# Performance work log

Measured on AMD Instinct MI355X. Metric: run time of the kernel, lower is better.

## Reference

```python
import jax, jax.numpy as jnp
import numpy as np

Q8 = 127.0   # 2**7 - 1
Q4 = 7.0     # 2**3 - 1
EPS = 1e-5
NEG = -1e9


def _quant_absmax_last(t, qmax=Q8):
    # smoothquant-style per-token / per-out-channel fake quant (clamp BEFORE div)
    scales = jnp.maximum(jnp.max(jnp.abs(t), axis=-1, keepdims=True), EPS) / qmax
    return jnp.round(t / scales) * scales


def _w8a8_linear(x, w, b, quantize_output=False):
    # W8A8Linear: 8-bit per-token act fake quant, 8-bit per-channel weight fake quant
    y = jnp.einsum('bte,oe->bto', _quant_absmax_last(x), _quant_absmax_last(w)) + b
    return _quant_absmax_last(y) if quantize_output else y


def _fake_quant_mix(t):
    # fake_quant_mix: xmax = abs().amax(-1, keepdim)[0] -> drops batch dim (uses batch-0 scales)
    xmax = jnp.max(jnp.abs(t), axis=-1, keepdims=True)[0]  # [T,1]
    scales = jnp.maximum(xmax / Q8, EPS)                   # clamp AFTER div here
    return jnp.round(t / scales) * scales


def _fake_quant_k4(t):
    # fake_quant: 4-bit, per last dim
    scales = jnp.maximum(jnp.max(jnp.abs(t), axis=-1, keepdims=True), EPS) / Q4
    return jnp.round(t / scales) * scales


def _fake_quant_v8(t):
    # fake_quant_v: 8-bit, axis=-2 (per channel over sequence)
    scales = jnp.maximum(jnp.max(jnp.abs(t), axis=-2, keepdims=True), EPS) / Q8
    return jnp.round(t / scales) * scales


def setup_inputs() -> dict:
    key = jax.random.key(0)
    ks = jax.random.split(key, 9)
    B, T, E = 1, 2048, 2048
    hidden_states = jax.random.normal(ks[0], (B, T, E), jnp.float32)
    causal = jnp.triu(jnp.full((T, T), NEG, jnp.float32), k=1)
    attention_mask = jnp.broadcast_to(causal[None, None], (B, 1, T, T))

    def lin(k):
        kw, kb = jax.random.split(k)
        w = jax.random.normal(kw, (E, E), jnp.float32) * (E ** -0.5)
        b = jax.random.normal(kb, (E,), jnp.float32) * 0.02
        return w, b

    q_w, q_b = lin(ks[1])
    k_w, k_b = lin(ks[2])
    v_w, v_b = lin(ks[3])
    o_w, o_b = lin(ks[4])
    return dict(hidden_states=hidden_states, attention_mask=attention_mask,
                q_w=q_w, q_b=q_b, k_w=k_w, k_b=k_b, v_w=v_w, v_b=v_b,
                o_w=o_w, o_b=o_b, num_heads=16)


def reference(hidden_states, attention_mask, q_w, q_b, k_w, k_b, v_w, v_b, o_w, o_b, num_heads):
    B, T, E = hidden_states.shape
    H = num_heads
    D = E // H
    scaling = D ** -0.5

    q = _w8a8_linear(hidden_states, q_w, q_b) * scaling                  # [B,T,E]
    k = _w8a8_linear(hidden_states, k_w, k_b)                            # [B,T,E]
    v = _w8a8_linear(hidden_states, v_w, v_b, quantize_output=True)      # [B,T,E]

    def to_heads(t):
        return t.reshape(B, T, H, D).transpose(0, 2, 1, 3).reshape(B * H, T, D)

    q1 = to_heads(q)
    k1 = to_heads(k)

    # ---- pass 1: heavy-hitter accumulated attention score ----
    aw = jnp.einsum('btd,bsd->bts', q1, k1)                               # [B*H,T,T]
    aw = aw.reshape(B, H, T, T) + attention_mask
    aw = jnp.maximum(aw, jnp.finfo(aw.dtype).min).reshape(B * H, T, T)
    tmp_attn = jax.nn.softmax(aw, axis=-1)
    acc = tmp_attn.sum(axis=-2).sum(axis=0)[None]                         # [1,T]
    heavy_budget = T
    row_vector = (heavy_budget - jnp.arange(heavy_budget, dtype=jnp.float32))[None]
    acc = acc / row_vector / (B * H)

    # grouped top-k over 4 equal score ranges
    ratios = [0.25, 0.25, 0.25, 0.25]
    k_top = int(heavy_budget / 40)
    idx_list = []
    start = 1
    for i, r in enumerate(ratios):
        rs = int(heavy_budget * r)
        end = min(start + rs - 1, heavy_budget) if i < len(ratios) - 1 else heavy_budget
        part = acc[:, start - 1:end]
        _, ti = jax.lax.top_k(part, k_top)
        idx_list.append(ti + (start - 1))
        start = end + 1
    topk_idx = jnp.concatenate(idx_list, axis=-1).reshape(-1)             # [4*k_top]

    # ---- mixed-precision KV fake quantization ----
    k_imp = _fake_quant_mix(k)        # 8-bit keys for important tokens
    k_low = _fake_quant_k4(k)         # 4-bit keys elsewhere
    k_mixed = k_low.at[:, topk_idx, :].set(k_imp[:, topk_idx, :])
    v_q = _fake_quant_v8(v)

    k2 = to_heads(k_mixed)
    v2 = to_heads(v_q)

    # ---- pass 2: real attention ----
    aw2 = jnp.einsum('btd,bsd->bts', q1, k2).reshape(B, H, T, T) + attention_mask
    probs = jax.nn.softmax(aw2.reshape(B * H, T, T), axis=-1)
    ctx = jnp.einsum('bts,bsd->btd', probs, v2)                           # [B*H,T,D]
    ctx = ctx.reshape(B, H, T, D).transpose(0, 2, 1, 3).reshape(B, T, E)
    return _w8a8_linear(ctx, o_w, o_b)
```

## Files before the change

kernel.cpp:

```cpp
#include <hip/hip_runtime.h>
#include <stdint.h>

#define TT 2048
#define EE 2048
#define HH 16
#define DD 128

static constexpr float F_EPS = 1e-5f;
static constexpr float F_SCALING = (float)0.08838834764831845;

using f32x4  = __attribute__((ext_vector_type(4))) float;
using bf16x8 = __attribute__((ext_vector_type(8))) short;
using u16x8  = __attribute__((ext_vector_type(8))) unsigned short;
using i32x4  = __attribute__((ext_vector_type(4))) int;

#define MFMA_BF16(a,b,c) __builtin_amdgcn_mfma_f32_16x16x32_bf16((a),(b),(c),0,0,0)
#define MFMA_I8(a,b,c)   __builtin_amdgcn_mfma_i32_16x16x64_i8((a),(b),(c),0,0,0)

#define GLD16(gp, lp) __builtin_amdgcn_global_load_lds( \
    (__attribute__((address_space(1))) void*)(unsigned long long)(gp), \
    (__attribute__((address_space(3))) void*)(lp), 16, 0, 0)

__device__ __forceinline__ unsigned short f2bf(float x){
  unsigned u = __float_as_uint(x);
  u = (u + 0x7FFFu + ((u >> 16) & 1u)) >> 16;
  return (unsigned short)u;
}
__device__ __forceinline__ float bf2f(unsigned short h){
  return __uint_as_float(((unsigned)h) << 16);
}
__device__ __forceinline__ float blockmax(float am, float* red, int tid){
  __syncthreads();
  #pragma unroll
  for (int o=1;o<64;o<<=1) am = fmaxf(am, __shfl_xor(am, o));
  if ((tid&63)==0) red[tid>>6] = am;
  __syncthreads();
  return fmaxf(fmaxf(red[0],red[1]), fmaxf(red[2],red[3]));
}

__device__ __forceinline__ void cid_map(int cid, int& qt, int& ch, int& nc){
  if (cid < 8)       { qt = cid;                ch = 0;            nc = 1; }
  else if (cid < 24) { qt = 8  + ((cid-8)>>1);  ch = (cid-8)&1;    nc = 2; }
  else if (cid < 48) { qt = 16 + (cid-24)/3;    ch = (cid-24)%3;   nc = 3; }
  else               { qt = 24 + ((cid-48)>>2); ch = (cid-48)&3;   nc = 4; }
}
__device__ __forceinline__ int aoff(int qt){
  return (qt<16) ? 2*(qt-8) : ((qt<24) ? 16+3*(qt-16) : 40+4*(qt-24));
}
__device__ __forceinline__ int aoff2(int qt){
  return (qt<16) ? (qt-8) : ((qt<24) ? 8+2*(qt-16) : 24+3*(qt-24));
}
__device__ __forceinline__ void attn_remap(int& h, int& cid){
  const int flat = blockIdx.y*80 + blockIdx.x;
  const int j = flat & 15;
  h = (j & 7)*2 + (j >> 3);
  cid = flat >> 4;
}

__device__ __forceinline__ void stage_k64x128(const unsigned short* gbase, unsigned short* lds, int tid){
  const char* gb = (const char*)gbase;
  char* lb = (char*)lds;
  #pragma unroll
  for (int i=0;i<4;i++){
    const int idx = i*256 + tid;
    const int r = idx >> 4, c = idx & 15;
    GLD16(gb + (size_t)r*(EE*2) + (unsigned)((c*16) ^ ((r&7)<<4)), lb + idx*16);
  }
}
__device__ __forceinline__ void stage_v128x64(const unsigned short* gbase, unsigned short* lds, int tid){
  const char* gb = (const char*)gbase;
  char* lb = (char*)lds;
  #pragma unroll
  for (int i=0;i<4;i++){
    const int idx = i*256 + tid;
    const int r = idx >> 3, c = idx & 7;
    GLD16(gb + (size_t)r*(TT*2) + (unsigned)((c*16) ^ ((r&7)<<4)), lb + idx*16);
  }
}
__device__ __forceinline__ bf16x8 frag_k(const unsigned short* lds, int kr, int dbyte){
  return *(const bf16x8*)((const char*)lds + kr*256 + (dbyte ^ ((kr&7)<<4)));
}
__device__ __forceinline__ bf16x8 frag_v(const unsigned short* lds, int dr, int kbyte){
  return *(const bf16x8*)((const char*)lds + dr*128 + (kbyte ^ ((dr&7)<<4)));
}

__global__ __launch_bounds__(256) void k_quant5(
    const float* __restrict__ hs, const float* __restrict__ qwf,
    const float* __restrict__ kwf, const float* __restrict__ vwf,
    const float* __restrict__ owf,
    char* __restrict__ qx, char* __restrict__ qw4,
    float* __restrict__ sx, float* __restrict__ sw)
{
  __shared__ float red[4];
  const int which = blockIdx.x >> 11;
  const int row = blockIdx.x & (TT-1);
  const int tid = threadIdx.x;
  const float* in; char* outq; float* outs;
  if      (which==0){ in=hs;  outq=qx;                   outs=sx;      }
  else if (which==1){ in=qwf; outq=qw4;                  outs=sw;      }
  else if (which==2){ in=kwf; outq=qw4+(size_t)EE*EE;    outs=sw+EE;   }
  else if (which==3){ in=vwf; outq=qw4+(size_t)2*EE*EE;  outs=sw+2*EE; }
  else              { in=owf; outq=qw4+(size_t)3*EE*EE;  outs=sw+3*EE; }
  const float* r = in + (size_t)row * EE;
  float x[8];
  {
    const f32x4 a = *(const f32x4*)(r + tid*8);
    const f32x4 b = *(const f32x4*)(r + tid*8 + 4);
    x[0]=a[0]; x[1]=a[1]; x[2]=a[2]; x[3]=a[3];
    x[4]=b[0]; x[5]=b[1]; x[6]=b[2]; x[7]=b[3];
  }
  float am = 0.f;
  #pragma unroll
  for (int j=0;j<8;j++) am = fmaxf(am, fabsf(x[j]));
  am = blockmax(am, red, tid);
  const float s = fmaxf(am, F_EPS) / 127.f;
  if (tid==0) outs[row] = s;
  union { char c[8]; int2 v; } u;
  #pragma unroll
  for (int j=0;j<8;j++) u.c[j] = (char)(int)rintf(x[j]/s);
  *(int2*)(outq + (size_t)row*EE + tid*8) = u.v;
}

__global__ __launch_bounds__(256) void k_rowquant8(
    const float* __restrict__ in, char* __restrict__ outq, float* __restrict__ outs)
{
  __shared__ float red[4];
  const int row = blockIdx.x;
  const int tid = threadIdx.x;
  const float* r = in + (size_t)row * EE;
  float x[8];
  {
    const f32x4 a = *(const f32x4*)(r + tid*8);
    const f32x4 b = *(const f32x4*)(r + tid*8 + 4);
    x[0]=a[0]; x[1]=a[1]; x[2]=a[2]; x[3]=a[3];
    x[4]=b[0]; x[5]=b[1]; x[6]=b[2]; x[7]=b[3];
  }
  float am = 0.f;
  #pragma unroll
  for (int j=0;j<8;j++) am = fmaxf(am, fabsf(x[j]));
  am = blockmax(am, red, tid);
  const float s = fmaxf(am, F_EPS) / 127.f;
  if (tid==0) outs[row] = s;
  union { char c[8]; int2 v; } u;
  #pragma unroll
  for (int j=0;j<8;j++) u.c[j] = (char)(int)rintf(x[j]/s);
  *(int2*)(outq + (size_t)row*EE + tid*8) = u.v;
}

__global__ __launch_bounds__(256) void k_quant_kmixed(
    const float* __restrict__ kin, const int* __restrict__ imp,
    unsigned short* __restrict__ qkm, float* __restrict__ sk,
    float* __restrict__ kmn)
{
  __shared__ float red[4];
  const int row = blockIdx.x;
  const int tid = threadIdx.x;
  const float* r = kin + (size_t)row * EE;
  float x[8];
  {
    const f32x4 a = *(const f32x4*)(r + tid*8);
    const f32x4 b = *(const f32x4*)(r + tid*8 + 4);
    x[0]=a[0]; x[1]=a[1]; x[2]=a[2]; x[3]=a[3];
    x[4]=b[0]; x[5]=b[1]; x[6]=b[2]; x[7]=b[3];
  }
  float am = 0.f;
  #pragma unroll
  for (int j=0;j<8;j++) am = fmaxf(am, fabsf(x[j]));
  am = blockmax(am, red, tid);
  float s;
  if (imp[row]) s = fmaxf(am / 127.f, F_EPS);
  else          s = fmaxf(am, F_EPS) / 7.f;
  if (tid==0) sk[row] = s;
  u16x8 qv;
  float ss = 0.f;
  #pragma unroll
  for (int j=0;j<8;j++){
    const float p = rintf(x[j]/s);
    qv[j] = f2bf(p);
    const float dq = p*s;
    ss += dq*dq;
  }
  *(u16x8*)(qkm + (size_t)row*EE + tid*8) = qv;
  ss += __shfl_xor(ss,1); ss += __shfl_xor(ss,2);
  ss += __shfl_xor(ss,4); ss += __shfl_xor(ss,8);
  const float mx = blockmax(ss, red, tid);
  if (tid==0) kmn[row] = __builtin_sqrtf(mx);
}

__global__ __launch_bounds__(256) void k_norm3(
    const unsigned short* __restrict__ qhi, const unsigned short* __restrict__ qlo,
    const float* __restrict__ kbuf, const float* __restrict__ vbuf,
    float* __restrict__ qn, float* __restrict__ kn, float* __restrict__ sdq)
{
  __shared__ float red[4];
  const int which = blockIdx.x >> 11;
  const int row = blockIdx.x & (TT-1);
  const int tid = threadIdx.x;
  if (which == 0){
    const u16x8 h = *(const u16x8*)(qhi + (size_t)row*EE + tid*8);
    const u16x8 l = *(const u16x8*)(qlo + (size_t)row*EE + tid*8);
    float ss = 0.f;
    #pragma unroll
    for (int j=0;j<8;j++){
      const float v = bf2f(h[j]) + bf2f(l[j]);
      ss += v*v;
    }
    ss += __shfl_xor(ss,1); ss += __shfl_xor(ss,2);
    ss += __shfl_xor(ss,4); ss += __shfl_xor(ss,8);
    const float mx = blockmax(ss, red, tid);
    if (tid==0) qn[row] = __builtin_sqrtf(mx);
  } else if (which == 1){
    const f32x4 a = *(const f32x4*)(kbuf + (size_t)row*EE + tid*8);
    const f32x4 b = *(const f32x4*)(kbuf + (size_t)row*EE + tid*8 + 4);
    float ss = a[0]*a[0]+a[1]*a[1]+a[2]*a[2]+a[3]*a[3]
             + b[0]*b[0]+b[1]*b[1]+b[2]*b[2]+b[3]*b[3];
    ss += __shfl_xor(ss,1); ss += __shfl_xor(ss,2);
    ss += __shfl_xor(ss,4); ss += __shfl_xor(ss,8);
    const float mx = blockmax(ss, red, tid);
    if (tid==0) kn[row] = __builtin_sqrtf(mx);
  } else {
    const f32x4 a = *(const f32x4*)(vbuf + (size_t)row*EE + tid*8);
    const f32x4 b = *(const f32x4*)(vbuf + (size_t)row*EE + tid*8 + 4);
    float am = fmaxf(fmaxf(fmaxf(fabsf(a[0]),fabsf(a[1])), fmaxf(fabsf(a[2]),fabsf(a[3]))),
                     fmaxf(fmaxf(fabsf(b[0]),fabsf(b[1])), fmaxf(fabsf(b[2]),fabsf(b[3]))));
    am = blockmax(am, red, tid);
    if (tid==0) sdq[row] = fmaxf(am, F_EPS) / 127.f;
  }
}

__global__ __launch_bounds__(256) void k_redmax2(
    const float* __restrict__ a, const float* __restrict__ b, float* __restrict__ dst)
{
  const float* s = blockIdx.x ? b : a;
  const int tid = threadIdx.x;
  float m = 0.f;
  #pragma unroll
  for (int i=0;i<8;i++) m = fmaxf(m, s[tid + i*256]);
  #pragma unroll
  for (int o=1;o<64;o<<=1) m = fmaxf(m, __shfl_xor(m,o));
  __shared__ float red[4];
  if ((tid&63)==0) red[tid>>6]=m;
  __syncthreads();
  if (tid==0) dst[blockIdx.x] = fmaxf(fmaxf(red[0],red[1]), fmaxf(red[2],red[3]));
}

__device__ __forceinline__ void gemm8_body(
    const char* __restrict__ Aq, const float* __restrict__ sa,
    const char* __restrict__ Bq, const float* __restrict__ sb,
    const float* __restrict__ bias, float post,
    float* __restrict__ Cout, unsigned short* __restrict__ Hout,
    unsigned short* __restrict__ Lout,
    char* lA, char* lB)
{
  const int tid = threadIdx.x;
  const int bm = blockIdx.y, bn = blockIdx.x;
  const int lane = tid & 63, w = tid >> 6;
  const int wr = w >> 1, wc = w & 1;
  i32x4 acc[4][2];
  const i32x4 IZ = {0,0,0,0};
  #pragma unroll
  for (int i=0;i<4;i++)
    #pragma unroll
    for (int j=0;j<2;j++) acc[i][j] = IZ;

  const char* gA = Aq + (size_t)(bm*128)*EE;
  const char* gB = Bq + (size_t)(bn*64)*EE;

  for (int k0 = 0; k0 < EE; k0 += 64) {
    #pragma unroll
    for (int i=0;i<2;i++){
      const int c = i*256 + tid;
      const int rr = c >> 2, k16 = c & 3;
      GLD16(gA + (size_t)rr*EE + k0 + ((k16*16) ^ (((rr>>1)&3)<<4)), lA + c*16);
    }
    {
      const int c = tid;
      const int rr = c >> 2, k16 = c & 3;
      GLD16(gB + (size_t)rr*EE + k0 + ((k16*16) ^ (((rr>>1)&3)<<4)), lB + c*16);
    }
    __syncthreads();
    i32x4 af[4], bf[2];
    #pragma unroll
    for (int mi=0;mi<4;mi++){
      const int rr = wr*64 + mi*16 + (lane&15);
      af[mi] = *(const i32x4*)(lA + rr*64 + (((lane>>4)*16) ^ (((rr>>1)&3)<<4)));
    }
    #pragma unroll
    for (int ni=0;ni<2;ni++){
      const int rr = wc*32 + ni*16 + (lane&15);
      bf[ni] = *(const i32x4*)(lB + rr*64 + (((lane>>4)*16) ^ (((rr>>1)&3)<<4)));
    }
    #pragma unroll
    for (int mi=0;mi<4;mi++)
      #pragma unroll
      for (int ni=0;ni<2;ni++)
        acc[mi][ni] = MFMA_I8(af[mi], bf[ni], acc[mi][ni]);
    __syncthreads();
  }
  const int row0 = bm*128 + wr*64;
  const int col0 = bn*64 + wc*32;
  #pragma unroll
  for (int mi=0;mi<4;mi++){
    #pragma unroll
    for (int r=0;r<4;r++){
      const int row = row0 + mi*16 + (lane>>4)*4 + r;
      const float sav = sa[row];
      #pragma unroll
      for (int ni=0;ni<2;ni++){
        const int col = col0 + ni*16 + (lane&15);
        const float v = ((float)acc[mi][ni][r]*sav*sb[col] + bias[col]) * post;
        if (Cout) Cout[(size_t)row*EE + col] = v;
        if (Hout){
          const unsigned short hh = f2bf(v);
          Hout[(size_t)row*EE + col] = hh;
          Lout[(size_t)row*EE + col] = f2bf(v - bf2f(hh));
        }
      }
    }
  }
}

__global__ __launch_bounds__(256) void k_gemm8_qkv(
    const char* __restrict__ Aq, const float* __restrict__ sa,
    const char* __restrict__ qw4, const float* __restrict__ sw,
    const float* __restrict__ q_b, const float* __restrict__ k_b,
    const float* __restrict__ v_b,
    float* __restrict__ kbuf, float* __restrict__ vbuf,
    unsigned short* __restrict__ q_hi, unsigned short* __restrict__ q_lo,
    unsigned short* __restrict__ k_hi, unsigned short* __restrict__ k_lo)
{
  __shared__ char lA[128*64];
  __shared__ char lB[64*64];
  const int z = blockIdx.z;
  const char* Bq = qw4 + (size_t)z*EE*EE;
  const float* sb = sw + z*EE;
  const float* bias = (z==0) ? q_b : (z==1) ? k_b : v_b;
  const float post = (z==0) ? F_SCALING : 1.f;
  float* Cout = (z==1) ? kbuf : (z==2) ? vbuf : nullptr;
  unsigned short* Hout = (z==0) ? q_hi : (z==1) ? k_hi : nullptr;
  unsigned short* Lout = (z==0) ? q_lo : (z==1) ? k_lo : nullptr;
  gemm8_body(Aq, sa, Bq, sb, bias, post, Cout, Hout, Lout, lA, lB);
}

__global__ __launch_bounds__(256) void k_gemm8_one(
    const char* __restrict__ Aq, const float* __restrict__ sa,
    const char* __restrict__ Bq, const float* __restrict__ sb,
    const float* __restrict__ bias, float* __restrict__ Cout)
{
  __shared__ char lA[128*64];
  __shared__ char lB[64*64];
  gemm8_body(Aq, sa, Bq, sb, bias, 1.f, Cout, nullptr, nullptr, lA, lB);
}

__global__ void k_init(unsigned* __restrict__ sv_bits, int* __restrict__ imp)
{
  const int i = blockIdx.x*256 + threadIdx.x;
  if (i < EE) sv_bits[i] = 0u;
  if (i < TT) imp[i] = 0;
}

__global__ __launch_bounds__(256) void k_colmax(
    const float* __restrict__ v, const float* __restrict__ sdq,
    unsigned* __restrict__ sv_bits)
{
  const int e = blockIdx.x*256 + threadIdx.x;
  const int t0 = blockIdx.y*64;
  float am = 0.f;
  for (int t=t0; t<t0+64; ++t){
    const float s = sdq[t];
    const float dq = rintf(v[(size_t)t*EE + e]/s)*s;
    am = fmaxf(am, fabsf(dq));
  }
  atomicMax(sv_bits + e, __float_as_uint(am));
}

__global__ __launch_bounds__(256) void k_vq_transpose(
    const float* __restrict__ v, const float* __restrict__ sdq,
    const unsigned* __restrict__ sv_bits,
    float* __restrict__ sv, unsigned short* __restrict__ qvT)
{
  __shared__ unsigned short tile[64][66];
  const int t0 = blockIdx.x*64, e0 = blockIdx.y*64;
  const int tid = threadIdx.x;
  {
    const int ee = tid & 63, tb = (tid>>6)*16;
    const float sve = fmaxf(__uint_as_float(sv_bits[e0+ee]), F_EPS) / 127.f;
    for (int i=0;i<16;i++){
      const int t = t0+tb+i;
      const float s = sdq[t];
      const float dq = rintf(v[(size_t)t*EE + e0+ee]/s)*s;
      tile[tb+i][ee] = f2bf(rintf(dq / sve));
    }
  }
  if (blockIdx.x==0 && tid<64)
    sv[e0+tid] = fmaxf(__uint_as_float(sv_bits[e0+tid]), F_EPS) / 127.f;
  __syncthreads();
  {
    const int ttl = tid & 63, ebl = (tid>>6)*16;
    for (int i=0;i<16;i++)
      qvT[(size_t)(e0+ebl+i)*TT + t0+ttl] = tile[ttl][ebl+i];
  }
}

__global__ __launch_bounds__(256) void k_attn1_stats(
    const unsigned short* __restrict__ qh, const unsigned short* __restrict__ ql,
    const unsigned short* __restrict__ kh, const unsigned short* __restrict__ kl,
    const float* __restrict__ nbv, float* __restrict__ lp)
{
  __shared__ unsigned short lKh[64*128];
  __shared__ unsigned short lKl[64*128];
  int h, cid; attn_remap(h, cid);
  int qt, ch, nc; cid_map(cid, qt, ch, nc);
  const int per = (qt + nc)/nc;
  const int s0 = ch*per, s1 = min(s0+per-1, qt);
  const int tid = threadIdx.x, w = tid>>6, lane = tid&63;
  const int row_base = qt*64 + w*16, lrow = (lane>>4)*4;
  const float B1 = nbv[0] * nbv[1] * 1.001f + 1e-3f;
  bf16x8 qhf[4], qlf[4];
  {
    const size_t qo = (size_t)(row_base + (lane&15))*EE + h*DD + (lane>>4)*8;
    #pragma unroll
    for (int kc=0;kc<4;kc++){
      qhf[kc] = *(const bf16x8*)(qh + qo + kc*32);
      qlf[kc] = *(const bf16x8*)(ql + qo + kc*32);
    }
  }
  float l_r[4] = {0.f,0.f,0.f,0.f};
  stage_k64x128(kh + (size_t)(s0*64)*EE + h*DD, lKh, tid);
  stage_k64x128(kl + (size_t)(s0*64)*EE + h*DD, lKl, tid);
  for (int st=s0; st<=s1; ++st){
    __syncthreads();
    f32x4 S[4];
    #pragma unroll
    for (int n=0;n<4;n++){
      f32x4 a = {0.f,0.f,0.f,0.f};
      const int kr = n*16 + (lane&15);
      #pragma unroll
      for (int kc=0;kc<4;kc++){
        const int db = kc*64 + (lane>>4)*16;
        const bf16x8 khf = frag_k(lKh, kr, db);
        const bf16x8 klf = frag_k(lKl, kr, db);
        a = MFMA_BF16(qhf[kc], khf, a);
        a = MFMA_BF16(qlf[kc], khf, a);
        a = MFMA_BF16(qhf[kc], klf, a);
      }
      S[n] = a;
    }
    __syncthreads();
    if (st < s1){
      stage_k64x128(kh + (size_t)((st+1)*64)*EE + h*DD, lKh, tid);
      stage_k64x128(kl + (size_t)((st+1)*64)*EE + h*DD, lKl, tid);
    }
    #pragma unroll
    for (int r=0;r<4;r++){
      const int row = row_base + lrow + r;
      float rs = 0.f;
      #pragma unroll
      for (int n=0;n<4;n++){
        const int col = st*64 + n*16 + (lane&15);
        rs += (col<=row) ? __expf(S[n][r]-B1) : 0.f;
      }
      rs += __shfl_xor(rs,1); rs += __shfl_xor(rs,2);
      rs += __shfl_xor(rs,4); rs += __shfl_xor(rs,8);
      l_r[r] += rs;
    }
  }
  if ((lane&15)==0){
    const int slot = (h*80 + cid)*64;
    #pragma unroll
    for (int r=0;r<4;r++)
      lp[slot + w*16 + lrow + r] = l_r[r];
  }
}

__global__ __launch_bounds__(64) void k_stats_combine(
    const float* __restrict__ lp, float* __restrict__ il1)
{
  const int qt = blockIdx.x, h = blockIdx.y, r = threadIdx.x;
  const int nc  = (qt<8)?1:((qt<16)?2:((qt<24)?3:4));
  const int off = (qt<8)?qt:((qt<16)?8+2*(qt-8):((qt<24)?24+3*(qt-16):48+4*(qt-24)));
  const int base = (h*80 + off)*64 + r;
  float l = 0.f;
  for (int i=0;i<nc;i++) l += lp[base + i*64];
  il1[h*TT + qt*64 + r] = 1.f/l;
}

__global__ __launch_bounds__(256) void k_attn1_acc(
    const unsigned short* __restrict__ qh, const unsigned short* __restrict__ ql,
    const unsigned short* __restrict__ kh, const unsigned short* __restrict__ kl,
    const float* __restrict__ nbv, const float* __restrict__ il1,
    float* __restrict__ partial)
{
  __shared__ unsigned short lKh[64*128];
  __shared__ unsigned short lKl[64*128];
  __shared__ float accw[4][512];
  int h, cid; attn_remap(h, cid);
  int qt, ch, nc; cid_map(cid, qt, ch, nc);
  const int per = (qt + nc)/nc;
  const int s0 = ch*per, s1 = min(s0+per-1, qt);
  const int tid = threadIdx.x, w = tid>>6, lane = tid&63;
  const int row_base = qt*64 + w*16, lrow = (lane>>4)*4;
  const float B1 = nbv[0] * nbv[1] * 1.001f + 1e-3f;
  bf16x8 qhf[4], qlf[4];
  {
    const size_t qo = (size_t)(row_base + (lane&15))*EE + h*DD + (lane>>4)*8;
    #pragma unroll
    for (int kc=0;kc<4;kc++){
      qhf[kc] = *(const bf16x8*)(qh + qo + kc*32);
      qlf[kc] = *(const bf16x8*)(ql + qo + kc*32);
    }
  }
  float il_r[4];
  #pragma unroll
  for (int r=0;r<4;r++)
    il_r[r] = il1[h*TT + row_base + lrow + r];
  stage_k64x128(kh + (size_t)(s0*64)*EE + h*DD, lKh, tid);
  stage_k64x128(kl + (size_t)(s0*64)*EE + h*DD, lKl, tid);
  for (int st=s0; st<=s1; ++st){
    __syncthreads();
    f32x4 S[4];
    #pragma unroll
    for (int n=0;n<4;n++){
      f32x4 a = {0.f,0.f,0.f,0.f};
      const int kr = n*16 + (lane&15);
      #pragma unroll
      for (int kc=0;kc<4;kc++){
        const int db = kc*64 + (lane>>4)*16;
        const bf16x8 khf = frag_k(lKh, kr, db);
        const bf16x8 klf = frag_k(lKl, kr, db);
        a = MFMA_BF16(qhf[kc], khf, a);
        a = MFMA_BF16(qlf[kc], khf, a);
        a = MFMA_BF16(qhf[kc], klf, a);
      }
      S[n] = a;
    }
    __syncthreads();
    if (st < s1){
      stage_k64x128(kh + (size_t)((st+1)*64)*EE + h*DD, lKh, tid);
      stage_k64x128(kl + (size_t)((st+1)*64)*EE + h*DD, lKl, tid);
    }
    #pragma unroll
    for (int n=0;n<4;n++){
      const int col = st*64 + n*16 + (lane&15);
      float cs = 0.f;
      #pragma unroll
      for (int r=0;r<4;r++){
        const int row = row_base + lrow + r;
        cs += (col<=row) ? __expf(S[n][r]-B1)*il_r[r] : 0.f;
      }
      cs += __shfl_xor(cs,16);
      cs += __shfl_xor(cs,32);
      if (lane < 16) accw[w][(st-s0)*64 + n*16 + lane] = cs;
    }
  }
  __syncthreads();
  const int ncols = (s1-s0+1)*64;
  float* dst = partial + (size_t)(h*32+qt)*TT + s0*64;
  for (int i=tid; i<ncols; i+=256)
    dst[i] = accw[0][i]+accw[1][i]+accw[2][i]+accw[3][i];
}

__global__ __launch_bounds__(256) void k_accsum(
    const float* __restrict__ partial, float* __restrict__ acc16)
{
  const int s = blockIdx.x*256 + threadIdx.x;
  const int hh = blockIdx.y;
  const int tmin = s >> 6;
  float a = 0.f;
  for (int qt=tmin; qt<32; ++qt)
    a += partial[(size_t)(hh*32+qt)*TT + s];
  acc16[hh*TT + s] = a;
}

__global__ __launch_bounds__(512) void k_select(
    const float* __restrict__ acc16, int* __restrict__ imp)
{
  __shared__ float vals[512];
  const int tid = threadIdx.x;
  const int s = blockIdx.x*512 + tid;
  float a = 0.f;
  #pragma unroll
  for (int hh=0; hh<16; ++hh) a += acc16[hh*TT + s];
  a = a / (float)(TT - s) / 16.f;
  vals[tid] = a;
  __syncthreads();
  int rank = 0;
  for (int j=0; j<512; ++j){
    const float vj = vals[j];
    rank += (vj > a) || (vj == a && j < tid);
  }
  imp[s] = (rank < 51) ? 1 : 0;
}

__global__ __launch_bounds__(256) void k_attn2(
    const unsigned short* __restrict__ qh, const unsigned short* __restrict__ ql,
    const unsigned short* __restrict__ qkm, const float* __restrict__ sk,
    const unsigned short* __restrict__ qvT, const float* __restrict__ sv,
    const float* __restrict__ nbv,
    float* __restrict__ ctx, float* __restrict__ lp2,
    unsigned short* __restrict__ Opart)
{
  __shared__ unsigned short lK[64*128];
  __shared__ unsigned short lV[128*64];
  __shared__ unsigned short Ph[4][16*64];
  int h, cid; attn_remap(h, cid);
  int qt, ch, nc; cid_map(cid, qt, ch, nc);
  const int per = (qt + nc)/nc;
  const int s0 = ch*per, s1 = min(s0+per-1, qt);
  const int tid = threadIdx.x, w = tid>>6, lane = tid&63;
  const int row_base = qt*64 + w*16, lrow = (lane>>4)*4;
  const float B2 = nbv[0] * nbv[2] * 1.001f + 1e-3f;
  bf16x8 qhf[4], qlf[4];
  {
    const size_t qo = (size_t)(row_base + (lane&15))*EE + h*DD + (lane>>4)*8;
    #pragma unroll
    for (int kc=0;kc<4;kc++){
      qhf[kc] = *(const bf16x8*)(qh + qo + kc*32);
      qlf[kc] = *(const bf16x8*)(ql + qo + kc*32);
    }
  }
  float l_r[4] = {0.f,0.f,0.f,0.f};
  f32x4 oa[8];
  const f32x4 FZ = {0.f,0.f,0.f,0.f};
  #pragma unroll
  for (int d8=0; d8<8; ++d8) oa[d8] = FZ;

  stage_k64x128(qkm + (size_t)(s0*64)*EE + h*DD, lK, tid);
  stage_v128x64(qvT + (size_t)(h*DD)*TT + s0*64, lV, tid);

  for (int st=s0; st<=s1; ++st){
    __syncthreads();
    f32x4 S[4];
    #pragma unroll
    for (int n=0;n<4;n++){
      f32x4 a = {0.f,0.f,0.f,0.f};
      const int kr = n*16 + (lane&15);
      #pragma unroll
      for (int kc=0;kc<4;kc++){
        const int db = kc*64 + (lane>>4)*16;
        const bf16x8 kf = frag_k(lK, kr, db);
        a = MFMA_BF16(qhf[kc], kf, a);
        a = MFMA_BF16(qlf[kc], kf, a);
      }
      S[n] = a * sk[st*64 + n*16 + (lane&15)];
    }
    #pragma unroll
    for (int r=0;r<4;r++){
      const int row = row_base + lrow + r;
      float rs = 0.f;
      #pragma unroll
      for (int n=0;n<4;n++){
        const int col = st*64 + n*16 + (lane&15);
        const float pv = (col<=row) ? __expf(S[n][r]-B2) : 0.f;
        rs += pv;
        *(unsigned short*)((char*)&Ph[w][0] + (lrow+r)*128 +
            ((((n*16 + (lane&15))*2)) ^ (((lrow+r)&7)<<4))) = f2bf(pv);
      }
      rs += __shfl_xor(rs,1); rs += __shfl_xor(rs,2);
      rs += __shfl_xor(rs,4); rs += __shfl_xor(rs,8);
      l_r[r] += rs;
    }
    bf16x8 pah[2];
    #pragma unroll
    for (int kc=0;kc<2;kc++){
      const int rr = lane&15;
      const int cb = kc*64 + (lane>>4)*16;
      pah[kc] = *(const bf16x8*)((const char*)&Ph[w][0] + rr*128 + (cb ^ ((rr&7)<<4)));
    }
    #pragma unroll
    for (int d8=0; d8<8; ++d8){
      const int dr = d8*16 + (lane&15);
      const int kb = (lane>>4)*16;
      const bf16x8 v0 = frag_v(lV, dr, kb);
      const bf16x8 v1 = frag_v(lV, dr, kb + 64);
      oa[d8] = MFMA_BF16(pah[0], v0, oa[d8]);
      oa[d8] = MFMA_BF16(pah[1], v1, oa[d8]);
    }
    __syncthreads();
    if (st < s1){
      stage_k64x128(qkm + (size_t)((st+1)*64)*EE + h*DD, lK, tid);
      stage_v128x64(qvT + (size_t)(h*DD)*TT + (st+1)*64, lV, tid);
    }
  }
  if (nc == 1){
    #pragma unroll
    for (int d8=0; d8<8; ++d8){
      const float sve = sv[h*DD + d8*16 + (lane&15)];
      #pragma unroll
      for (int r=0;r<4;r++){
        const int row = row_base + lrow + r;
        ctx[(size_t)row*EE + h*DD + d8*16 + (lane&15)] = oa[d8][r]*sve/l_r[r];
      }
    }
  } else {
    const int slotl = h*72 + aoff(qt) + ch;
    if ((lane&15)==0){
      #pragma unroll
      for (int r=0;r<4;r++)
        lp2[slotl*64 + w*16 + lrow + r] = l_r[r];
    }
    if (ch == 0){
      #pragma unroll
      for (int d8=0; d8<8; ++d8){
        #pragma unroll
        for (int r=0;r<4;r++){
          const int row = row_base + lrow + r;
          ctx[(size_t)row*EE + h*DD + d8*16 + (lane&15)] = oa[d8][r];
        }
      }
    } else {
      const int slot = h*48 + aoff2(qt) + (ch-1);
      #pragma unroll
      for (int d8=0; d8<8; ++d8){
        #pragma unroll
        for (int r=0;r<4;r++)
          Opart[(size_t)slot*8192 + (w*16 + lrow + r)*128 + d8*16 + (lane&15)] = f2bf(oa[d8][r]);
      }
    }
  }
}

__global__ __launch_bounds__(256) void k_attn2_combine(
    const float* __restrict__ lp2,
    const unsigned short* __restrict__ Opart, const float* __restrict__ sv,
    float* __restrict__ ctx)
{
  __shared__ float lst[64];
  const int qt = 8 + blockIdx.x, h = blockIdx.y;
  const int nc = (qt + 8) >> 3;
  const int basel = h*72 + aoff(qt);
  const int baseo = h*48 + aoff2(qt);
  const int tid = threadIdx.x;
  if (tid < 64){
    float l = 0.f;
    for (int i=0;i<nc;i++) l += lp2[(basel+i)*64 + tid];
    lst[tid] = 1.f/l;
  }
  __syncthreads();
  #pragma unroll
  for (int e=0;e<32;e++){
    const int idx = e*256 + tid;
    const int row = idx>>7, d = idx&127;
    float a = ctx[(size_t)(qt*64+row)*EE + h*DD + d];
    for (int i=0;i<nc-1;i++)
      a += bf2f(Opart[(size_t)(baseo+i)*8192 + idx]);
    ctx[(size_t)(qt*64+row)*EE + h*DD + d] = a * sv[h*DD + d] * lst[row];
  }
}

extern "C" void kernel_launch(void* const* d_in, const int* in_sizes, int n_in,
                              void* d_out, int out_size, void* d_ws, size_t ws_size,
                              hipStream_t stream)
{
  (void)in_sizes; (void)n_in; (void)out_size; (void)ws_size;
  const float* hs  = (const float*)d_in[0];
  const float* q_w = (const float*)d_in[2];
  const float* q_b = (const float*)d_in[3];
  const float* k_w = (const float*)d_in[4];
  const float* k_b = (const float*)d_in[5];
  const float* v_w = (const float*)d_in[6];
  const float* v_b = (const float*)d_in[7];
  const float* o_w = (const float*)d_in[8];
  const float* o_b = (const float*)d_in[9];

  char* ws = (char*)d_ws;
  const size_t MB = 1ull<<20;
  char*           qx   = (char*)(ws + 0*MB);
  char*           qw4  = (char*)(ws + 4*MB);
  unsigned short* q_hi = (unsigned short*)(ws + 20*MB);
  unsigned short* q_lo = (unsigned short*)(ws + 28*MB);
  float*          kbuf = (float*)(ws + 36*MB);
  unsigned short* k_hi = (unsigned short*)(ws + 52*MB);
  unsigned short* k_lo = (unsigned short*)(ws + 60*MB);
  float*          vbuf = (float*)(ws + 68*MB);
  unsigned short* qvT  = (unsigned short*)(ws + 84*MB);
  char*           sm   = ws + 92*MB;
  float*    sx   = (float*)(sm + 0);
  float*    sw   = (float*)(sm + 8*1024);
  float*    sdq  = (float*)(sm + 40*1024);
  float*    il1  = (float*)(sm + 48*1024);
  int*      imp  = (int*)(sm + 176*1024);
  float*    skv  = (float*)(sm + 184*1024);
  unsigned* sv_bits = (unsigned*)(sm + 192*1024);
  float*    sv   = (float*)(sm + 200*1024);
  float*    sctx = (float*)(sm + 208*1024);
  float*    nbv  = (float*)(sm + 216*1024);
  float*    qn_row = (float*)(sm + 224*1024);
  float*    kn_row = (float*)(sm + 232*1024);
  float*    kmn_row= (float*)(sm + 240*1024);
  float* lp  = (float*)qx;
  float* acc16 = (float*)qw4;
  float* partial = (float*)vbuf;
  unsigned short* Opart = (unsigned short*)vbuf;
  float* lp2 = (float*)(ws + 81*MB);
  unsigned short* qkm  = k_hi;
  float*          ctx  = kbuf;
  char*           qctx = qx;

  dim3 b256(256);
  dim3 ga(80, HH);

  k_init<<<8, b256, 0, stream>>>(sv_bits, imp);
  k_quant5<<<5*TT, b256, 0, stream>>>(hs, q_w, k_w, v_w, o_w, qx, qw4, sx, sw);
  k_gemm8_qkv<<<dim3(EE/64, TT/128, 3), b256, 0, stream>>>(
      qx, sx, qw4, sw, q_b, k_b, v_b, kbuf, vbuf, q_hi, q_lo, k_hi, k_lo);
  k_norm3<<<3*TT, b256, 0, stream>>>(q_hi, q_lo, kbuf, vbuf, qn_row, kn_row, sdq);
  k_redmax2<<<2, b256, 0, stream>>>(qn_row, kn_row, nbv);
  k_colmax<<<dim3(EE/256, TT/64), b256, 0, stream>>>(vbuf, sdq, sv_bits);
  k_vq_transpose<<<dim3(TT/64, EE/64), b256, 0, stream>>>(vbuf, sdq, sv_bits, sv, qvT);
  k_attn1_stats<<<ga, b256, 0, stream>>>(q_hi, q_lo, k_hi, k_lo, nbv, lp);
  k_stats_combine<<<dim3(32,16), dim3(64), 0, stream>>>(lp, il1);
  k_attn1_acc<<<ga, b256, 0, stream>>>(q_hi, q_lo, k_hi, k_lo, nbv, il1, partial);
  k_accsum<<<dim3(TT/256, HH), b256, 0, stream>>>(partial, acc16);
  k_select<<<4, dim3(512), 0, stream>>>(acc16, imp);
  k_quant_kmixed<<<TT, b256, 0, stream>>>(kbuf, imp, qkm, skv, kmn_row);
  k_redmax2<<<1, b256, 0, stream>>>(kmn_row, kmn_row, nbv + 2);
  k_attn2<<<ga, b256, 0, stream>>>(q_hi, q_lo, qkm, skv, qvT, sv, nbv, ctx, lp2, Opart);
  k_attn2_combine<<<dim3(24,16), b256, 0, stream>>>(lp2, Opart, sv, ctx);
  k_rowquant8<<<TT, b256, 0, stream>>>(ctx, qctx, sctx);
  k_gemm8_one<<<dim3(EE/64, TT/128), b256, 0, stream>>>(
      qctx, sctx, qw4 + (size_t)3*EE*EE, sw + 3*EE, o_b, (float*)d_out);
}
```

Baseline: 337.3 us.

## Double-buffer K/V LDS tiles in attention kernels to overlap loads with compute

Result: slower. 346.8 us (+2.8%).

```diff
diff --git a/kernel.cpp b/kernel.cpp
--- a/kernel.cpp
+++ b/kernel.cpp
@@ -407,8 +407,10 @@
     const unsigned short* __restrict__ kh, const unsigned short* __restrict__ kl,
     const float* __restrict__ nbv, float* __restrict__ lp)
 {
-  __shared__ unsigned short lKh[64*128];
-  __shared__ unsigned short lKl[64*128];
+  __shared__ unsigned short lKhA[64*128];
+  __shared__ unsigned short lKlA[64*128];
+  __shared__ unsigned short lKhB[64*128];
+  __shared__ unsigned short lKlB[64*128];
   int h, cid; attn_remap(h, cid);
   int qt, ch, nc; cid_map(cid, qt, ch, nc);
   const int per = (qt + nc)/nc;
@@ -416,6 +418,9 @@
   const int tid = threadIdx.x, w = tid>>6, lane = tid&63;
   const int row_base = qt*64 + w*16, lrow = (lane>>4)*4;
   const float B1 = nbv[0] * nbv[1] * 1.001f + 1e-3f;
+  unsigned short *curKh = lKhA, *curKl = lKlA, *nxtKh = lKhB, *nxtKl = lKlB;
+  stage_k64x128(kh + (size_t)(s0*64)*EE + h*DD, curKh, tid);
+  stage_k64x128(kl + (size_t)(s0*64)*EE + h*DD, curKl, tid);
   bf16x8 qhf[4], qlf[4];
   {
     const size_t qo = (size_t)(row_base + (lane&15))*EE + h*DD + (lane>>4)*8;
@@ -426,10 +431,12 @@
     }
   }
   float l_r[4] = {0.f,0.f,0.f,0.f};
-  stage_k64x128(kh + (size_t)(s0*64)*EE + h*DD, lKh, tid);
-  stage_k64x128(kl + (size_t)(s0*64)*EE + h*DD, lKl, tid);
   for (int st=s0; st<=s1; ++st){
     __syncthreads();
+    if (st < s1){
+      stage_k64x128(kh + (size_t)((st+1)*64)*EE + h*DD, nxtKh, tid);
+      stage_k64x128(kl + (size_t)((st+1)*64)*EE + h*DD, nxtKl, tid);
+    }
     f32x4 S[4];
     #pragma unroll
     for (int n=0;n<4;n++){
@@ -438,19 +445,14 @@
       #pragma unroll
       for (int kc=0;kc<4;kc++){
         const int db = kc*64 + (lane>>4)*16;
-        const bf16x8 khf = frag_k(lKh, kr, db);
-        const bf16x8 klf = frag_k(lKl, kr, db);
+        const bf16x8 khf = frag_k(curKh, kr, db);
+        const bf16x8 klf = frag_k(curKl, kr, db);
         a = MFMA_BF16(qhf[kc], khf, a);
         a = MFMA_BF16(qlf[kc], khf, a);
         a = MFMA_BF16(qhf[kc], klf, a);
       }
       S[n] = a;
     }
-    __syncthreads();
-    if (st < s1){
-      stage_k64x128(kh + (size_t)((st+1)*64)*EE + h*DD, lKh, tid);
-      stage_k64x128(kl + (size_t)((st+1)*64)*EE + h*DD, lKl, tid);
-    }
     #pragma unroll
     for (int r=0;r<4;r++){
       const int row = row_base + lrow + r;
@@ -464,6 +466,9 @@
       rs += __shfl_xor(rs,4); rs += __shfl_xor(rs,8);
       l_r[r] += rs;
     }
+    unsigned short* t;
+    t = curKh; curKh = nxtKh; nxtKh = t;
+    t = curKl; curKl = nxtKl; nxtKl = t;
   }
   if ((lane&15)==0){
     const int slot = (h*80 + cid)*64;
@@ -491,8 +496,10 @@
     const float* __restrict__ nbv, const float* __restrict__ il1,
     float* __restrict__ partial)
 {
-  __shared__ unsigned short lKh[64*128];
-  __shared__ unsigned short lKl[64*128];
+  __shared__ unsigned short lKhA[64*128];
+  __shared__ unsigned short lKlA[64*128];
+  __shared__ unsigned short lKhB[64*128];
+  __shared__ unsigned short lKlB[64*128];
   __shared__ float accw[4][512];
   int h, cid; attn_remap(h, cid);
   int qt, ch, nc; cid_map(cid, qt, ch, nc);
@@ -501,6 +508,9 @@
   const int tid = threadIdx.x, w = tid>>6, lane = tid&63;
   const int row_base = qt*64 + w*16, lrow = (lane>>4)*4;
   const float B1 = nbv[0] * nbv[1] * 1.001f + 1e-3f;
+  unsigned short *curKh = lKhA, *curKl = lKlA, *nxtKh = lKhB, *nxtKl = lKlB;
+  stage_k64x128(kh + (size_t)(s0*64)*EE + h*DD, curKh, tid);
+  stage_k64x128(kl + (size_t)(s0*64)*EE + h*DD, curKl, tid);
   bf16x8 qhf[4], qlf[4];
   {
     const size_t qo = (size_t)(row_base + (lane&15))*EE + h*DD + (lane>>4)*8;
@@ -514,10 +524,12 @@
   #pragma unroll
   for (int r=0;r<4;r++)
     il_r[r] = il1[h*TT + row_base + lrow + r];
-  stage_k64x128(kh + (size_t)(s0*64)*EE + h*DD, lKh, tid);
-  stage_k64x128(kl + (size_t)(s0*64)*EE + h*DD, lKl, tid);
   for (int st=s0; st<=s1; ++st){
     __syncthreads();
+    if (st < s1){
+      stage_k64x128(kh + (size_t)((st+1)*64)*EE + h*DD, nxtKh, tid);
+      stage_k64x128(kl + (size_t)((st+1)*64)*EE + h*DD, nxtKl, tid);
+    }
     f32x4 S[4];
     #pragma unroll
     for (int n=0;n<4;n++){
@@ -526,19 +538,14 @@
       #pragma unroll
       for (int kc=0;kc<4;kc++){
         const int db = kc*64 + (lane>>4)*16;
-        const bf16x8 khf = frag_k(lKh, kr, db);
-        const bf16x8 klf = frag_k(lKl, kr, db);
+        const bf16x8 khf = frag_k(curKh, kr, db);
+        const bf16x8 klf = frag_k(curKl, kr, db);
         a = MFMA_BF16(qhf[kc], khf, a);
         a = MFMA_BF16(qlf[kc], khf, a);
         a = MFMA_BF16(qhf[kc], klf, a);
       }
       S[n] = a;
     }
-    __syncthreads();
-    if (st < s1){
-      stage_k64x128(kh + (size_t)((st+1)*64)*EE + h*DD, lKh, tid);
-      stage_k64x128(kl + (size_t)((st+1)*64)*EE + h*DD, lKl, tid);
-    }
     #pragma unroll
     for (int n=0;n<4;n++){
       const int col = st*64 + n*16 + (lane&15);
@@ -552,6 +559,9 @@
       cs += __shfl_xor(cs,32);
       if (lane < 16) accw[w][(st-s0)*64 + n*16 + lane] = cs;
     }
+    unsigned short* t;
+    t = curKh; curKh = nxtKh; nxtKh = t;
+    t = curKl; curKl = nxtKl; nxtKl = t;
   }
   __syncthreads();
   const int ncols = (s1-s0+1)*64;
@@ -600,8 +610,10 @@
     float* __restrict__ ctx, float* __restrict__ lp2,
     unsigned short* __restrict__ Opart)
 {
-  __shared__ unsigned short lK[64*128];
-  __shared__ unsigned short lV[128*64];
+  __shared__ unsigned short lKA[64*128];
+  __shared__ unsigned short lVA[128*64];
+  __shared__ unsigned short lKB[64*128];
+  __shared__ unsigned short lVB[128*64];
   __shared__ unsigned short Ph[4][16*64];
   int h, cid; attn_remap(h, cid);
   int qt, ch, nc; cid_map(cid, qt, ch, nc);
@@ -610,6 +622,9 @@
   const int tid = threadIdx.x, w = tid>>6, lane = tid&63;
   const int row_base = qt*64 + w*16, lrow = (lane>>4)*4;
   const float B2 = nbv[0] * nbv[2] * 1.001f + 1e-3f;
+  unsigned short *curK = lKA, *curV = lVA, *nxtK = lKB, *nxtV = lVB;
+  stage_k64x128(qkm + (size_t)(s0*64)*EE + h*DD, curK, tid);
+  stage_v128x64(qvT + (size_t)(h*DD)*TT + s0*64, curV, tid);
   bf16x8 qhf[4], qlf[4];
   {
     const size_t qo = (size_t)(row_base + (lane&15))*EE + h*DD + (lane>>4)*8;
@@ -625,11 +640,12 @@
   #pragma unroll
   for (int d8=0; d8<8; ++d8) oa[d8] = FZ;
 
-  stage_k64x128(qkm + (size_t)(s0*64)*EE + h*DD, lK, tid);
-  stage_v128x64(qvT + (size_t)(h*DD)*TT + s0*64, lV, tid);
-
   for (int st=s0; st<=s1; ++st){
     __syncthreads();
+    if (st < s1){
+      stage_k64x128(qkm + (size_t)((st+1)*64)*EE + h*DD, nxtK, tid);
+      stage_v128x64(qvT + (size_t)(h*DD)*TT + (st+1)*64, nxtV, tid);
+    }
     f32x4 S[4];
     #pragma unroll
     for (int n=0;n<4;n++){
@@ -638,7 +654,7 @@
       #pragma unroll
       for (int kc=0;kc<4;kc++){
         const int db = kc*64 + (lane>>4)*16;
-        const bf16x8 kf = frag_k(lK, kr, db);
+        const bf16x8 kf = frag_k(curK, kr, db);
         a = MFMA_BF16(qhf[kc], kf, a);
         a = MFMA_BF16(qlf[kc], kf, a);
       }
@@ -671,16 +687,14 @@
     for (int d8=0; d8<8; ++d8){
       const int dr = d8*16 + (lane&15);
       const int kb = (lane>>4)*16;
-      const bf16x8 v0 = frag_v(lV, dr, kb);
-      const bf16x8 v1 = frag_v(lV, dr, kb + 64);
+      const bf16x8 v0 = frag_v(curV, dr, kb);
+      const bf16x8 v1 = frag_v(curV, dr, kb + 64);
       oa[d8] = MFMA_BF16(pah[0], v0, oa[d8]);
       oa[d8] = MFMA_BF16(pah[1], v1, oa[d8]);
     }
-    __syncthreads();
-    if (st < s1){
-      stage_k64x128(qkm + (size_t)((st+1)*64)*EE + h*DD, lK, tid);
-      stage_v128x64(qvT + (size_t)(h*DD)*TT + (st+1)*64, lV, tid);
-    }
+    unsigned short* t;
+    t = curK; curK = nxtK; nxtK = t;
+    t = curV; curV = nxtV; nxtV = t;
   }
   if (nc == 1){
     #pragma unroll
```

## Enlarge int8 GEMM tile to 128x128 and double-buffer K/V in attention

Applied to the files above, without the earlier changes.

Result: faster. 321.2 us (-4.8%).

```diff
diff --git a/kernel.cpp b/kernel.cpp
--- a/kernel.cpp
+++ b/kernel.cpp
@@ -256,15 +256,15 @@
   const int bm = blockIdx.y, bn = blockIdx.x;
   const int lane = tid & 63, w = tid >> 6;
   const int wr = w >> 1, wc = w & 1;
-  i32x4 acc[4][2];
+  i32x4 acc[4][4];
   const i32x4 IZ = {0,0,0,0};
   #pragma unroll
   for (int i=0;i<4;i++)
     #pragma unroll
-    for (int j=0;j<2;j++) acc[i][j] = IZ;
+    for (int j=0;j<4;j++) acc[i][j] = IZ;
 
   const char* gA = Aq + (size_t)(bm*128)*EE;
-  const char* gB = Bq + (size_t)(bn*64)*EE;
+  const char* gB = Bq + (size_t)(bn*128)*EE;
 
   for (int k0 = 0; k0 < EE; k0 += 64) {
     #pragma unroll
@@ -273,32 +273,33 @@
       const int rr = c >> 2, k16 = c & 3;
       GLD16(gA + (size_t)rr*EE + k0 + ((k16*16) ^ (((rr>>1)&3)<<4)), lA + c*16);
     }
-    {
-      const int c = tid;
+    #pragma unroll
+    for (int i=0;i<2;i++){
+      const int c = i*256 + tid;
       const int rr = c >> 2, k16 = c & 3;
       GLD16(gB + (size_t)rr*EE + k0 + ((k16*16) ^ (((rr>>1)&3)<<4)), lB + c*16);
     }
     __syncthreads();
-    i32x4 af[4], bf[2];
+    i32x4 af[4], bf[4];
     #pragma unroll
     for (int mi=0;mi<4;mi++){
       const int rr = wr*64 + mi*16 + (lane&15);
       af[mi] = *(const i32x4*)(lA + rr*64 + (((lane>>4)*16) ^ (((rr>>1)&3)<<4)));
     }
     #pragma unroll
-    for (int ni=0;ni<2;ni++){
-      const int rr = wc*32 + ni*16 + (lane&15);
+    for (int ni=0;ni<4;ni++){
+      const int rr = wc*64 + ni*16 + (lane&15);
       bf[ni] = *(const i32x4*)(lB + rr*64 + (((lane>>4)*16) ^ (((rr>>1)&3)<<4)));
     }
     #pragma unroll
     for (int mi=0;mi<4;mi++)
       #pragma unroll
-      for (int ni=0;ni<2;ni++)
+      for (int ni=0;ni<4;ni++)
         acc[mi][ni] = MFMA_I8(af[mi], bf[ni], acc[mi][ni]);
     __syncthreads();
   }
   const int row0 = bm*128 + wr*64;
-  const int col0 = bn*64 + wc*32;
+  const int col0 = bn*128 + wc*64;
   #pragma unroll
   for (int mi=0;mi<4;mi++){
     #pragma unroll
@@ -306,7 +307,7 @@
       const int row = row0 + mi*16 + (lane>>4)*4 + r;
       const float sav = sa[row];
       #pragma unroll
-      for (int ni=0;ni<2;ni++){
+      for (int ni=0;ni<4;ni++){
         const int col = col0 + ni*16 + (lane&15);
         const float v = ((float)acc[mi][ni][r]*sav*sb[col] + bias[col]) * post;
         if (Cout) Cout[(size_t)row*EE + col] = v;
@@ -330,7 +331,7 @@
     unsigned short* __restrict__ k_hi, unsigned short* __restrict__ k_lo)
 {
   __shared__ char lA[128*64];
-  __shared__ char lB[64*64];
+  __shared__ char lB[128*64];
   const int z = blockIdx.z;
   const char* Bq = qw4 + (size_t)z*EE*EE;
   const float* sb = sw + z*EE;
@@ -348,7 +349,7 @@
     const float* __restrict__ bias, float* __restrict__ Cout)
 {
   __shared__ char lA[128*64];
-  __shared__ char lB[64*64];
+  __shared__ char lB[128*64];
   gemm8_body(Aq, sa, Bq, sb, bias, 1.f, Cout, nullptr, nullptr, lA, lB);
 }
 
@@ -600,8 +601,10 @@
     float* __restrict__ ctx, float* __restrict__ lp2,
     unsigned short* __restrict__ Opart)
 {
-  __shared__ unsigned short lK[64*128];
-  __shared__ unsigned short lV[128*64];
+  __shared__ unsigned short lKA[64*128];
+  __shared__ unsigned short lVA[128*64];
+  __shared__ unsigned short lKB[64*128];
+  __shared__ unsigned short lVB[128*64];
   __shared__ unsigned short Ph[4][16*64];
   int h, cid; attn_remap(h, cid);
   int qt, ch, nc; cid_map(cid, qt, ch, nc);
@@ -610,6 +613,9 @@
   const int tid = threadIdx.x, w = tid>>6, lane = tid&63;
   const int row_base = qt*64 + w*16, lrow = (lane>>4)*4;
   const float B2 = nbv[0] * nbv[2] * 1.001f + 1e-3f;
+  unsigned short *curK = lKA, *curV = lVA, *nxtK = lKB, *nxtV = lVB;
+  stage_k64x128(qkm + (size_t)(s0*64)*EE + h*DD, curK, tid);
+  stage_v128x64(qvT + (size_t)(h*DD)*TT + s0*64, curV, tid);
   bf16x8 qhf[4], qlf[4];
   {
     const size_t qo = (size_t)(row_base + (lane&15))*EE + h*DD + (lane>>4)*8;
@@ -625,11 +631,12 @@
   #pragma unroll
   for (int d8=0; d8<8; ++d8) oa[d8] = FZ;
 
-  stage_k64x128(qkm + (size_t)(s0*64)*EE + h*DD, lK, tid);
-  stage_v128x64(qvT + (size_t)(h*DD)*TT + s0*64, lV, tid);
-
   for (int st=s0; st<=s1; ++st){
     __syncthreads();
+    if (st < s1){
+      stage_k64x128(qkm + (size_t)((st+1)*64)*EE + h*DD, nxtK, tid);
+      stage_v128x64(qvT + (size_t)(h*DD)*TT + (st+1)*64, nxtV, tid);
+    }
     f32x4 S[4];
     #pragma unroll
     for (int n=0;n<4;n++){
@@ -638,7 +645,7 @@
       #pragma unroll
       for (int kc=0;kc<4;kc++){
         const int db = kc*64 + (lane>>4)*16;
-        const bf16x8 kf = frag_k(lK, kr, db);
+        const bf16x8 kf = frag_k(curK, kr, db);
         a = MFMA_BF16(qhf[kc], kf, a);
         a = MFMA_BF16(qlf[kc], kf, a);
       }
@@ -671,16 +678,14 @@
     for (int d8=0; d8<8; ++d8){
       const int dr = d8*16 + (lane&15);
       const int kb = (lane>>4)*16;
-      const bf16x8 v0 = frag_v(lV, dr, kb);
-      const bf16x8 v1 = frag_v(lV, dr, kb + 64);
+      const bf16x8 v0 = frag_v(curV, dr, kb);
+      const bf16x8 v1 = frag_v(curV, dr, kb + 64);
       oa[d8] = MFMA_BF16(pah[0], v0, oa[d8]);
       oa[d8] = MFMA_BF16(pah[1], v1, oa[d8]);
     }
-    __syncthreads();
-    if (st < s1){
-      stage_k64x128(qkm + (size_t)((st+1)*64)*EE + h*DD, lK, tid);
-      stage_v128x64(qvT + (size_t)(h*DD)*TT + (st+1)*64, lV, tid);
-    }
+    unsigned short* t;
+    t = curK; curK = nxtK; nxtK = t;
+    t = curV; curV = nxtV; nxtV = t;
   }
   if (nc == 1){
     #pragma unroll
@@ -802,7 +807,7 @@
 
   k_init<<<8, b256, 0, stream>>>(sv_bits, imp);
   k_quant5<<<5*TT, b256, 0, stream>>>(hs, q_w, k_w, v_w, o_w, qx, qw4, sx, sw);
-  k_gemm8_qkv<<<dim3(EE/64, TT/128, 3), b256, 0, stream>>>(
+  k_gemm8_qkv<<<dim3(EE/128, TT/128, 3), b256, 0, stream>>>(
       qx, sx, qw4, sw, q_b, k_b, v_b, kbuf, vbuf, q_hi, q_lo, k_hi, k_lo);
   k_norm3<<<3*TT, b256, 0, stream>>>(q_hi, q_lo, kbuf, vbuf, qn_row, kn_row, sdq);
   k_redmax2<<<2, b256, 0, stream>>>(qn_row, kn_row, nbv);
@@ -818,6 +823,6 @@
   k_attn2<<<ga, b256, 0, stream>>>(q_hi, q_lo, qkm, skv, qvT, sv, nbv, ctx, lp2, Opart);
   k_attn2_combine<<<dim3(24,16), b256, 0, stream>>>(lp2, Opart, sv, ctx);
   k_rowquant8<<<TT, b256, 0, stream>>>(ctx, qctx, sctx);
-  k_gemm8_one<<<dim3(EE/64, TT/128), b256, 0, stream>>>(
+  k_gemm8_one<<<dim3(EE/128, TT/128), b256, 0, stream>>>(
       qctx, sctx, qw4 + (size_t)3*EE*EE, sw + 3*EE, o_b, (float*)d_out);
 }
```
